# Kernel tuning notes

Measured on AMD Instinct MI355X. Metric: run time of the kernel, lower is better.

## Reference

```python
import jax, jax.numpy as jnp
import numpy as np

B = 32768

def setup_inputs() -> dict:
    key = jax.random.key(0)
    ks = jax.random.split(key, 6)
    x = jax.random.normal(ks[0], (B, 1, 28, 28), dtype=jnp.float32)
    conv_w = jax.random.normal(ks[1], (4, 1, 2, 2), dtype=jnp.float32) * 0.5   # Conv2d(1,4,2,2) OIHW
    conv_b = jax.random.normal(ks[2], (4,), dtype=jnp.float32) * 0.1
    q_w = jax.random.normal(ks[3], (4, 4), dtype=jnp.float32) * 0.5            # Linear(4,4,bias=False), (out,in)
    lin_w = jax.random.normal(ks[4], (10, 1568), dtype=jnp.float32) * 0.02     # Linear(1568,10), (out,in)
    lin_b = jax.random.normal(ks[5], (10,), dtype=jnp.float32) * 0.02
    return {"x": x, "conv_w": conv_w, "conv_b": conv_b, "q_w": q_w, "lin_w": lin_w, "lin_b": lin_b}

def reference(x, conv_w, conv_b, q_w, lin_w, lin_b):
    b = x.shape[0]
    # conv branch: (B,1,28,28) -> (B,4,14,14)
    conv = jax.lax.conv_general_dilated(
        x, conv_w, window_strides=(2, 2), padding='VALID',
        dimension_numbers=('NCHW', 'OIHW', 'NCHW')) + conv_b[None, :, None, None]
    cls_feat = conv.reshape(b, -1)  # (B,784)
    # quantum branch: all 196 non-overlapping 2x2 patches in loop (r,c) order,
    # each flattened row-major to 4 values, then one batched 4x4 linear.
    img = x.reshape(b, 28, 28)
    patches = img.reshape(b, 14, 2, 14, 2).transpose(0, 1, 3, 2, 4).reshape(b, 196, 4)
    qfeat = jnp.einsum('bpi,oi->bpo', patches, q_w).reshape(b, 196 * 4)  # (B,784)
    combined = jnp.concatenate([cls_feat, qfeat], axis=1)  # (B,1568)
    logits = combined @ lin_w.T + lin_b
    return jax.nn.log_softmax(logits, axis=-1)
```

## Files before the change

### kernel.cpp

```cpp
#include <hip/hip_runtime.h>
#include <math.h>

#define NOUT   10
#define ROWLEN 784
#define WTOT   (NOUT*ROWLEN)

__global__ __launch_bounds__(256, 4)
void quanv_fused(const float* __restrict__ x,
                 const float* __restrict__ conv_w,
                 const float* __restrict__ conv_b,
                 const float* __restrict__ q_w,
                 const float* __restrict__ lin_w,
                 const float* __restrict__ lin_b,
                 float* __restrict__ out)
{
    __shared__ float Wl[WTOT];
    __shared__ float bias[NOUT];
    __shared__ float rs[40];

    const int t = threadIdx.x;

    {
        const int lane = t & 7;
        for (int pair = t >> 3; pair < 40; pair += 32) {
            const int o = pair >> 2, c = pair & 3;
            const float* base = lin_w + o * 1568 + c * 196;
            float s = 0.f;
            #pragma unroll
            for (int p = 0; p < 196; p += 8) {
                const int pp = p + lane;
                if (pp < 196) s += base[pp];
            }
            s += __shfl_xor(s, 1);
            s += __shfl_xor(s, 2);
            s += __shfl_xor(s, 4);
            if (lane == 0) rs[pair] = s;
        }
    }

    for (int idx = t; idx < WTOT; idx += 256) {
        const int o = idx / ROWLEN;
        const int j = idx - o * ROWLEN;
        const int h = j / 28, w = j - h * 28;
        const int p = (h >> 1) * 14 + (w >> 1);
        const int k = (h & 1) * 2 + (w & 1);
        float s = 0.f;
        #pragma unroll
        for (int c = 0; c < 4; ++c)
            s += conv_w[c * 4 + k] * lin_w[o * 1568 + c * 196 + p];
        #pragma unroll
        for (int q = 0; q < 4; ++q)
            s += q_w[q * 4 + k] * lin_w[o * 1568 + 784 + p * 4 + q];
        Wl[idx] = s;
    }

    __syncthreads();
    if (t < NOUT) {
        float s = lin_b[t];
        #pragma unroll
        for (int c = 0; c < 4; ++c) s += conv_b[c] * rs[t * 4 + c];
        bias[t] = s;
    }
    __syncthreads();

    const int l  = t & 15;
    const int g  = t >> 4;
    const int r0 = blockIdx.x * 32 + 2 * g;

    const float* __restrict__ xr0 = x + (size_t)r0 * ROWLEN;
    const float* __restrict__ xr1 = xr0 + ROWLEN;

    float acc0[NOUT], acc1[NOUT];
    #pragma unroll
    for (int o = 0; o < NOUT; ++o) { acc0[o] = 0.f; acc1[o] = 0.f; }

    float4 a = *(const float4*)(xr0 + 4 * l);
    float4 b = *(const float4*)(xr1 + 4 * l);

    #pragma unroll 3
    for (int i = 0; i < 12; ++i) {
        float4 an, bn;
        if (i < 11) {
            const int nfo = 4 * l + 64 * (i + 1);
            an = *(const float4*)(xr0 + nfo);
            bn = *(const float4*)(xr1 + nfo);
        } else {
            const int tfo = 768 + 4 * (l & 3);
            an = *(const float4*)(xr0 + tfo);
            bn = *(const float4*)(xr1 + tfo);
        }
        const int fo = 4 * l + 64 * i;
        #pragma unroll
        for (int o = 0; o < NOUT; ++o) {
            const float4 wv = *(const float4*)&Wl[o * ROWLEN + fo];
            acc0[o] = fmaf(a.x, wv.x, fmaf(a.y, wv.y, fmaf(a.z, wv.z, fmaf(a.w, wv.w, acc0[o]))));
            acc1[o] = fmaf(b.x, wv.x, fmaf(b.y, wv.y, fmaf(b.z, wv.z, fmaf(b.w, wv.w, acc1[o]))));
        }
        a = an; b = bn;
    }
    if (l < 4) {
        const int fo = 768 + 4 * l;
        #pragma unroll
        for (int o = 0; o < NOUT; ++o) {
            const float4 wv = *(const float4*)&Wl[o * ROWLEN + fo];
            acc0[o] = fmaf(a.x, wv.x, fmaf(a.y, wv.y, fmaf(a.z, wv.z, fmaf(a.w, wv.w, acc0[o]))));
            acc1[o] = fmaf(b.x, wv.x, fmaf(b.y, wv.y, fmaf(b.z, wv.z, fmaf(b.w, wv.w, acc1[o]))));
        }
    }

    #pragma unroll
    for (int o = 0; o < NOUT; ++o) {
        acc0[o] += __shfl_xor(acc0[o], 1);
        acc0[o] += __shfl_xor(acc0[o], 2);
        acc0[o] += __shfl_xor(acc0[o], 4);
        acc0[o] += __shfl_xor(acc0[o], 8);
        acc1[o] += __shfl_xor(acc1[o], 1);
        acc1[o] += __shfl_xor(acc1[o], 2);
        acc1[o] += __shfl_xor(acc1[o], 4);
        acc1[o] += __shfl_xor(acc1[o], 8);
    }

    float lg0[NOUT], lg1[NOUT];
    float m0 = -1e30f, m1 = -1e30f;
    #pragma unroll
    for (int o = 0; o < NOUT; ++o) {
        lg0[o] = acc0[o] + bias[o]; m0 = fmaxf(m0, lg0[o]);
        lg1[o] = acc1[o] + bias[o]; m1 = fmaxf(m1, lg1[o]);
    }
    float s0 = 0.f, s1 = 0.f;
    #pragma unroll
    for (int o = 0; o < NOUT; ++o) {
        s0 += expf(lg0[o] - m0);
        s1 += expf(lg1[o] - m1);
    }
    const float lse0 = m0 + logf(s0);
    const float lse1 = m1 + logf(s1);

    if (l < NOUT) {
        float v0 = lg0[0], v1 = lg1[0];
        #pragma unroll
        for (int o = 1; o < NOUT; ++o) {
            v0 = (l == o) ? lg0[o] : v0;
            v1 = (l == o) ? lg1[o] : v1;
        }
        out[(size_t)r0 * NOUT + l]       = v0 - lse0;
        out[(size_t)(r0 + 1) * NOUT + l] = v1 - lse1;
    }
}

extern "C" void kernel_launch(void* const* d_in, const int* in_sizes, int n_in,
                              void* d_out, int out_size, void* d_ws, size_t ws_size,
                              hipStream_t stream) {
    const float* x      = (const float*)d_in[0];
    const float* conv_w = (const float*)d_in[1];
    const float* conv_b = (const float*)d_in[2];
    const float* q_w    = (const float*)d_in[3];
    const float* lin_w  = (const float*)d_in[4];
    const float* lin_b  = (const float*)d_in[5];
    float* out = (float*)d_out;

    const int rows = in_sizes[0] / ROWLEN;
    quanv_fused<<<rows / 32, 256, 0, stream>>>(x, conv_w, conv_b, q_w,
                                               lin_w, lin_b, out);
}
```

Before: 38.44 us.

## Precompute folded weights in a prep kernel and deepen x prefetch

The per-block folding of conv and quantum weights into the 10x784 linear weight moves into a separate prep kernel that writes them once to workspace. The main kernel then just copies the folded weights into shared memory with float4 loads, instead of every one of the 1024 blocks recomputing them from scattered global reads. The x-row loads now prefetch two iterations ahead using alternating register buffers, with the loop fully unrolled. The cost is an extra kernel launch plus a serial dependency, and higher register pressure.

Measured after the change: 32.23 us. -16.2%, faster.

```diff
diff --git a/kernel.cpp b/kernel.cpp
--- a/kernel.cpp
+++ b/kernel.cpp
@@ -5,22 +5,34 @@
 #define ROWLEN 784
 #define WTOT   (NOUT*ROWLEN)
 
-__global__ __launch_bounds__(256, 4)
-void quanv_fused(const float* __restrict__ x,
-                 const float* __restrict__ conv_w,
-                 const float* __restrict__ conv_b,
-                 const float* __restrict__ q_w,
-                 const float* __restrict__ lin_w,
-                 const float* __restrict__ lin_b,
-                 float* __restrict__ out)
+__global__ __launch_bounds__(256)
+void quanv_prep(const float* __restrict__ conv_w,
+                const float* __restrict__ conv_b,
+                const float* __restrict__ q_w,
+                const float* __restrict__ lin_w,
+                const float* __restrict__ lin_b,
+                float* __restrict__ W)
 {
-    __shared__ float Wl[WTOT];
-    __shared__ float bias[NOUT];
-    __shared__ float rs[40];
-
     const int t = threadIdx.x;
 
-    {
+    for (int idx = blockIdx.x * 256 + t; idx < WTOT; idx += gridDim.x * 256) {
+        const int o = idx / ROWLEN;
+        const int j = idx - o * ROWLEN;
+        const int h = j / 28, w = j - h * 28;
+        const int p = (h >> 1) * 14 + (w >> 1);
+        const int k = (h & 1) * 2 + (w & 1);
+        float s = 0.f;
+        #pragma unroll
+        for (int c = 0; c < 4; ++c)
+            s += conv_w[c * 4 + k] * lin_w[o * 1568 + c * 196 + p];
+        #pragma unroll
+        for (int q = 0; q < 4; ++q)
+            s += q_w[q * 4 + k] * lin_w[o * 1568 + 784 + p * 4 + q];
+        W[idx] = s;
+    }
+
+    if (blockIdx.x == 0) {
+        __shared__ float rs[40];
         const int lane = t & 7;
         for (int pair = t >> 3; pair < 40; pair += 32) {
             const int o = pair >> 2, c = pair & 3;
@@ -36,33 +48,37 @@
             s += __shfl_xor(s, 4);
             if (lane == 0) rs[pair] = s;
         }
+        __syncthreads();
+        if (t < NOUT) {
+            float s = lin_b[t];
+            #pragma unroll
+            for (int c = 0; c < 4; ++c) s += conv_b[c] * rs[t * 4 + c];
+            W[WTOT + t] = s;
+        }
     }
+}
 
-    for (int idx = t; idx < WTOT; idx += 256) {
-        const int o = idx / ROWLEN;
-        const int j = idx - o * ROWLEN;
-        const int h = j / 28, w = j - h * 28;
-        const int p = (h >> 1) * 14 + (w >> 1);
-        const int k = (h & 1) * 2 + (w & 1);
-        float s = 0.f;
+__global__ __launch_bounds__(256, 4)
+void quanv_main(const float* __restrict__ x,
+                const float* __restrict__ Wg,
+                float* __restrict__ out)
+{
+    __shared__ float Wl[WTOT];
+    __shared__ float bias[NOUT];
+
+    {
+        const float4* __restrict__ src = (const float4*)Wg;
+        float4* dst = (float4*)Wl;
         #pragma unroll
-        for (int c = 0; c < 4; ++c)
-            s += conv_w[c * 4 + k] * lin_w[o * 1568 + c * 196 + p];
-        #pragma unroll
-        for (int q = 0; q < 4; ++q)
-            s += q_w[q * 4 + k] * lin_w[o * 1568 + 784 + p * 4 + q];
-        Wl[idx] = s;
-    }
-
-    __syncthreads();
-    if (t < NOUT) {
-        float s = lin_b[t];
-        #pragma unroll
-        for (int c = 0; c < 4; ++c) s += conv_b[c] * rs[t * 4 + c];
-        bias[t] = s;
+        for (int i = 0; i < 8; ++i) {
+            const int idx = threadIdx.x + 256 * i;
+            if (idx < WTOT / 4) dst[idx] = src[idx];
+        }
+        if (threadIdx.x < NOUT) bias[threadIdx.x] = Wg[WTOT + threadIdx.x];
     }
     __syncthreads();
 
+    const int t  = threadIdx.x;
     const int l  = t & 15;
     const int g  = t >> 4;
     const int r0 = blockIdx.x * 32 + 2 * g;
@@ -74,21 +90,32 @@
     #pragma unroll
     for (int o = 0; o < NOUT; ++o) { acc0[o] = 0.f; acc1[o] = 0.f; }
 
-    float4 a = *(const float4*)(xr0 + 4 * l);
-    float4 b = *(const float4*)(xr1 + 4 * l);
+    float4 pa0 = *(const float4*)(xr0 + 4 * l);
+    float4 pb0 = *(const float4*)(xr1 + 4 * l);
+    float4 pa1 = *(const float4*)(xr0 + 4 * l + 64);
+    float4 pb1 = *(const float4*)(xr1 + 4 * l + 64);
 
-    #pragma unroll 3
+    #pragma unroll
     for (int i = 0; i < 12; ++i) {
-        float4 an, bn;
-        if (i < 11) {
-            const int nfo = 4 * l + 64 * (i + 1);
-            an = *(const float4*)(xr0 + nfo);
-            bn = *(const float4*)(xr1 + nfo);
-        } else {
+        float4 a, b;
+        if ((i & 1) == 0) { a = pa0; b = pb0; } else { a = pa1; b = pb1; }
+
+        const int ni = i + 2;
+        if (ni < 12) {
+            const int nfo = 4 * l + 64 * ni;
+            if ((i & 1) == 0) {
+                pa0 = *(const float4*)(xr0 + nfo);
+                pb0 = *(const float4*)(xr1 + nfo);
+            } else {
+                pa1 = *(const float4*)(xr0 + nfo);
+                pb1 = *(const float4*)(xr1 + nfo);
+            }
+        } else if (ni == 12) {
             const int tfo = 768 + 4 * (l & 3);
-            an = *(const float4*)(xr0 + tfo);
-            bn = *(const float4*)(xr1 + tfo);
+            pa0 = *(const float4*)(xr0 + tfo);
+            pb0 = *(const float4*)(xr1 + tfo);
         }
+
         const int fo = 4 * l + 64 * i;
         #pragma unroll
         for (int o = 0; o < NOUT; ++o) {
@@ -96,15 +123,14 @@
             acc0[o] = fmaf(a.x, wv.x, fmaf(a.y, wv.y, fmaf(a.z, wv.z, fmaf(a.w, wv.w, acc0[o]))));
             acc1[o] = fmaf(b.x, wv.x, fmaf(b.y, wv.y, fmaf(b.z, wv.z, fmaf(b.w, wv.w, acc1[o]))));
         }
-        a = an; b = bn;
     }
     if (l < 4) {
         const int fo = 768 + 4 * l;
         #pragma unroll
         for (int o = 0; o < NOUT; ++o) {
             const float4 wv = *(const float4*)&Wl[o * ROWLEN + fo];
-            acc0[o] = fmaf(a.x, wv.x, fmaf(a.y, wv.y, fmaf(a.z, wv.z, fmaf(a.w, wv.w, acc0[o]))));
-            acc1[o] = fmaf(b.x, wv.x, fmaf(b.y, wv.y, fmaf(b.z, wv.z, fmaf(b.w, wv.w, acc1[o]))));
+            acc0[o] = fmaf(pa0.x, wv.x, fmaf(pa0.y, wv.y, fmaf(pa0.z, wv.z, fmaf(pa0.w, wv.w, acc0[o]))));
+            acc1[o] = fmaf(pb0.x, wv.x, fmaf(pb0.y, wv.y, fmaf(pb0.z, wv.z, fmaf(pb0.w, wv.w, acc1[o]))));
         }
     }
 
@@ -158,8 +184,10 @@
     const float* lin_w  = (const float*)d_in[4];
     const float* lin_b  = (const float*)d_in[5];
     float* out = (float*)d_out;
+    float* W   = (float*)d_ws;
 
     const int rows = in_sizes[0] / ROWLEN;
-    quanv_fused<<<rows / 32, 256, 0, stream>>>(x, conv_w, conv_b, q_w,
-                                               lin_w, lin_b, out);
+
+    quanv_prep<<<31, 256, 0, stream>>>(conv_w, conv_b, q_w, lin_w, lin_b, W);
+    quanv_main<<<rows / 32, 256, 0, stream>>>(x, W, out);
 }
```
